# Kernel optimization log

Measured on AMD Instinct MI355X. Metric: run time of the kernel, lower is better.

Reference implementation:

```python
import jax, jax.numpy as jnp
import numpy as np

N_HEADS = 8
N_FILTERS = 512
HEAD_DIM = N_FILTERS // N_HEADS  # key_dim == value_dim == 64
BATCH = 32
SEQ = 4096


def setup_inputs() -> dict:
    key = jax.random.key(0)
    ks = jax.random.split(key, 9)
    s_in = 1.0 / np.sqrt(N_FILTERS)
    s_out = 1.0 / np.sqrt(N_HEADS * HEAD_DIM)
    return {
        "x": jax.random.normal(ks[0], (BATCH, SEQ, N_FILTERS), dtype=jnp.float32),
        # stacked per-head projection weights, stored as [H, in, out]
        "Wq": jax.random.uniform(ks[1], (N_HEADS, N_FILTERS, HEAD_DIM), jnp.float32, -s_in, s_in),
        "bq": jax.random.uniform(ks[2], (N_HEADS, HEAD_DIM), jnp.float32, -s_in, s_in),
        "Wk": jax.random.uniform(ks[3], (N_HEADS, N_FILTERS, HEAD_DIM), jnp.float32, -s_in, s_in),
        "bk": jax.random.uniform(ks[4], (N_HEADS, HEAD_DIM), jnp.float32, -s_in, s_in),
        "Wv": jax.random.uniform(ks[5], (N_HEADS, N_FILTERS, HEAD_DIM), jnp.float32, -s_in, s_in),
        "bv": jax.random.uniform(ks[6], (N_HEADS, HEAD_DIM), jnp.float32, -s_in, s_in),
        "Wo": jax.random.uniform(ks[7], (N_HEADS * HEAD_DIM, N_FILTERS), jnp.float32, -s_out, s_out),
        "bo": jax.random.uniform(ks[8], (N_FILTERS,), jnp.float32, -s_out, s_out),
    }


def reference(x, Wq, bq, Wk, bk, Wv, bv, Wo, bo):
    B, L, F = x.shape
    # Per-head projections, batched over heads: [H, B, L, D]
    Q = jnp.einsum("blf,hfd->hbld", x, Wq) + bq[:, None, None, :]
    K = jnp.einsum("blf,hfd->hbld", x, Wk) + bk[:, None, None, :]
    V = jnp.einsum("blf,hfd->hbld", x, Wv) + bv[:, None, None, :]
    # Feature-space attention: Q^T K -> [H, B, D, D], scale, softmax over dim=1 (rows)
    scores = jnp.einsum("hbld,hble->hbde", Q, K) / np.sqrt(HEAD_DIM).astype(np.float32)
    A = jax.nn.softmax(scores, axis=-2)
    # heads[i] = V @ A : [H, B, L, D]
    heads = jnp.einsum("hbld,hbde->hble", V, A)
    # Faithful to torch: heads.view(batch, l, -1) reinterprets the [H,B,L,D] buffer
    out = heads.reshape(B, L, N_HEADS * HEAD_DIM)
    return out @ Wo + bo
```

## Files before the change

kernel.cpp:

```cpp
#include <hip/hip_runtime.h>
#include <hip/hip_bf16.h>
#include <cstdint>
#include <cstddef>

#define BATCH 32
#define SEQ   4096
#define NF    512
#define NH    8
#define HD    64

typedef __bf16 bf16x8 __attribute__((ext_vector_type(8)));
typedef __bf16 bf16x4 __attribute__((ext_vector_type(4)));
typedef float  f32x4  __attribute__((ext_vector_type(4)));

__device__ __forceinline__ int lds_off(int m, int kg) {
  return (((m >> 4) * 4 + kg) * 16 + (m & 15)) * 8;
}

template<int MODE>
struct SRegs { bf16x8 h0, h1, l0, l1; };

__device__ __forceinline__ void cvt8(const float* f, bf16x8& vh, bf16x8& vl) {
#pragma unroll
  for (int j = 0; j < 8; ++j) {
    float x = f[j];
    __bf16 h = (__bf16)x;
    vh[j] = h;
    vl[j] = (__bf16)(x - (float)h);
  }
}

template<int MODE>
__device__ __forceinline__ SRegs<MODE> stage_load(
    const void* pa, const void* pb, long long zoff, int ld,
    long long row0, int k0, int tid)
{
  SRegs<MODE> R;
  if constexpr (MODE == 0 || MODE == 3) {
    const __bf16* hi = (const __bf16*)pa + zoff;
    const int r = tid >> 1, half = tid & 1;
    const size_t base = (size_t)(row0 + r) * ld + k0 + half * 16;
    R.h0 = *(const bf16x8*)(hi + base);
    R.h1 = *(const bf16x8*)(hi + base + 8);
    if constexpr (MODE == 0) {
      const __bf16* lo = (const __bf16*)pb + zoff;
      R.l0 = *(const bf16x8*)(lo + base);
      R.l1 = *(const bf16x8*)(lo + base + 8);
    }
  } else if constexpr (MODE == 1 || MODE == 4) {
    const float* A = (const float*)pa + zoff;
    const int r = tid >> 1, half = tid & 1;
    const float* src = A + (size_t)(row0 + r) * ld + k0 + half * 16;
    float f[16];
#pragma unroll
    for (int q = 0; q < 4; ++q) {
      float4 v = *(const float4*)&src[q * 4];
      f[q * 4 + 0] = v.x; f[q * 4 + 1] = v.y; f[q * 4 + 2] = v.z; f[q * 4 + 3] = v.w;
    }
    if constexpr (MODE == 1) {
      cvt8(f, R.h0, R.l0);
      cvt8(f + 8, R.h1, R.l1);
    } else {
#pragma unroll
      for (int j = 0; j < 8; ++j) {
        R.h0[j] = (__bf16)f[j];
        R.h1[j] = (__bf16)f[8 + j];
      }
    }
  } else {
    const float* A = (const float*)pa + zoff;
    const int m = tid & 127, lg = (tid >> 7) * 16;
    float f[16];
#pragma unroll
    for (int i = 0; i < 16; ++i)
      f[i] = A[(size_t)(k0 + lg + i) * ld + row0 + m];
    cvt8(f, R.h0, R.l0);
    cvt8(f + 8, R.h1, R.l1);
  }
  return R;
}

template<int MODE>
__device__ __forceinline__ void stage_store(
    const SRegs<MODE>& R, __bf16* sH, __bf16* sL, int tid)
{
  if constexpr (MODE == 2) {
    const int m = tid & 127, kq = (tid >> 7) * 2;
    *(bf16x8*)&sH[lds_off(m, kq + 0)] = R.h0;
    *(bf16x8*)&sH[lds_off(m, kq + 1)] = R.h1;
    *(bf16x8*)&sL[lds_off(m, kq + 0)] = R.l0;
    *(bf16x8*)&sL[lds_off(m, kq + 1)] = R.l1;
  } else {
    const int r = tid >> 1, kq = (tid & 1) * 2;
    *(bf16x8*)&sH[lds_off(r, kq + 0)] = R.h0;
    *(bf16x8*)&sH[lds_off(r, kq + 1)] = R.h1;
    if constexpr (MODE == 0 || MODE == 1) {
      *(bf16x8*)&sL[lds_off(r, kq + 0)] = R.l0;
      *(bf16x8*)&sL[lds_off(r, kq + 1)] = R.l1;
    }
  }
}

template<int MA, int MB, int EPI, bool SYM = false>
__global__ __launch_bounds__(256) void mfma_nt(
    const void* Aa, const void* Ab, long long sA, int lda,
    const void* Ba, const void* Bb, long long sB, int ldb,
    const float* __restrict__ bias, void* C0, void* C1, long long sC, int K)
{
  constexpr bool AL = (MA <= 2);
  constexpr bool BL = (MB <= 2);
  constexpr int NBUF = 2 + (AL ? 1 : 0) + (BL ? 1 : 0);
  __shared__ __bf16 smem[NBUF * 4096];
  __bf16* sAh = smem;
  __bf16* sBh = smem + 4096;
  __bf16* sAl = AL ? (smem + 8192) : smem;
  __bf16* sBl = BL ? (smem + (AL ? 12288 : 8192)) : smem;

  const int tid = threadIdx.x;
  const int lane = tid & 63, wave = tid >> 6;
  const int wm = wave >> 1, wn = wave & 1;

  const unsigned nx = gridDim.x, ny = gridDim.y;
  const unsigned nwg = nx * ny * gridDim.z;
  unsigned bid = blockIdx.x + nx * (blockIdx.y + ny * blockIdx.z);
  unsigned nid = (bid & 7) * (nwg >> 3) + (bid >> 3);
  const unsigned bx = nid % nx;
  unsigned t = nid / nx;
  const unsigned by = t % ny;
  const unsigned z = t / ny;

  unsigned ti = 0, tj = 0;
  long long m0;
  int n0;
  if constexpr (SYM) {
    if (bx < 4)      { ti = 0; tj = bx; }
    else if (bx < 7) { ti = 1; tj = bx - 3; }
    else if (bx < 9) { ti = 2; tj = bx - 5; }
    else             { ti = 3; tj = 3; }
    m0 = (long long)ti * 128;
    n0 = tj * 128;
  } else {
    m0 = (long long)by * 128;
    n0 = bx * 128;
  }
  const long long zA = (long long)z * sA, zB = (long long)z * sB;

  f32x4 acc[4][4];
#pragma unroll
  for (int i = 0; i < 4; ++i)
#pragma unroll
    for (int j = 0; j < 4; ++j)
#pragma unroll
      for (int c = 0; c < 4; ++c) acc[i][j][c] = 0.f;

  const int kg = lane >> 4, r = lane & 15;

  SRegs<MA> ra = stage_load<MA>(Aa, Ab, zA, lda, m0, 0, tid);
  SRegs<MB> rb = stage_load<MB>(Ba, Bb, zB, ldb, n0, 0, tid);

  for (int k0 = 0; k0 < K; k0 += 32) {
    __syncthreads();
    stage_store<MA>(ra, sAh, sAl, tid);
    stage_store<MB>(rb, sBh, sBl, tid);
    __syncthreads();
    if (k0 + 32 < K) {
      ra = stage_load<MA>(Aa, Ab, zA, lda, m0, k0 + 32, tid);
      rb = stage_load<MB>(Ba, Bb, zB, ldb, n0, k0 + 32, tid);
    }

    bf16x8 ah[4], al[4], bh[4], bl[4];
#pragma unroll
    for (int i = 0; i < 4; ++i) {
      ah[i] = *(const bf16x8*)&sAh[lds_off(wm * 64 + i * 16 + r, kg)];
      if constexpr (AL)
        al[i] = *(const bf16x8*)&sAl[lds_off(wm * 64 + i * 16 + r, kg)];
      bh[i] = *(const bf16x8*)&sBh[lds_off(wn * 64 + i * 16 + r, kg)];
      if constexpr (BL)
        bl[i] = *(const bf16x8*)&sBl[lds_off(wn * 64 + i * 16 + r, kg)];
    }
#pragma unroll
    for (int i = 0; i < 4; ++i)
#pragma unroll
      for (int j = 0; j < 4; ++j) {
        acc[i][j] = __builtin_amdgcn_mfma_f32_16x16x32_bf16(ah[i], bh[j], acc[i][j], 0, 0, 0);
        if constexpr (AL)
          acc[i][j] = __builtin_amdgcn_mfma_f32_16x16x32_bf16(al[i], bh[j], acc[i][j], 0, 0, 0);
        if constexpr (BL)
          acc[i][j] = __builtin_amdgcn_mfma_f32_16x16x32_bf16(ah[i], bl[j], acc[i][j], 0, 0, 0);
      }
  }

  const int rbase = (lane >> 4) * 4;
  const int cn = lane & 15;
#pragma unroll
  for (int i = 0; i < 4; ++i) {
    const long long gm = m0 + wm * 64 + i * 16 + rbase;
#pragma unroll
    for (int j = 0; j < 4; ++j) {
      const int gn = n0 + wn * 64 + j * 16 + cn;
      if constexpr (EPI == 0) {
        float* C = (float*)C0 + (long long)z * sC;
#pragma unroll
        for (int rr = 0; rr < 4; ++rr)
          C[(size_t)(gm + rr) * 512 + gn] = acc[i][j][rr];
      } else if constexpr (EPI == 1) {
        float* C = (float*)C0;
        const float bv = bias[gn];
#pragma unroll
        for (int rr = 0; rr < 4; ++rr)
          C[(size_t)(gm + rr) * 512 + gn] = acc[i][j][rr] + bv;
      } else if constexpr (EPI == 2) {
        __bf16* Ch = (__bf16*)C0 + (long long)z * sC;
        __bf16* Cl = (__bf16*)C1 + (long long)z * sC;
        bf16x4 th, tl;
#pragma unroll
        for (int rr = 0; rr < 4; ++rr) {
          float v = acc[i][j][rr];
          __bf16 h = (__bf16)v;
          th[rr] = h;
          tl[rr] = (__bf16)(v - (float)h);
          Ch[(size_t)(gm + rr) * 512 + gn] = h;
          Cl[(size_t)(gm + rr) * 512 + gn] = tl[rr];
        }
        if constexpr (SYM) {
          if (ti != tj) {
            *(bf16x4*)&Ch[(size_t)gn * 512 + gm] = th;
            *(bf16x4*)&Cl[(size_t)gn * 512 + gm] = tl;
          }
        }
      } else {
        const int h = gn >> 6, e = gn & 63;
        const float bv = bias[(h * 32 + (int)z) * 64 + e];
        __bf16* Ch = (__bf16*)C0;
        const size_t rowb = (size_t)(h * 32 + (int)z) * 4096 + gm;
#pragma unroll
        for (int rr = 0; rr < 4; ++rr)
          Ch[(rowb + rr) * 64 + e] = (__bf16)(acc[i][j][rr] + bv);
      }
    }
  }
}

__global__ void pack3_kernel(const float* __restrict__ Wq, const float* __restrict__ Wk,
                             const float* __restrict__ Wv, const float* __restrict__ Wo,
                             float* __restrict__ Wq_all, float* __restrict__ Wk_all,
                             float* __restrict__ Wv_all,
                             __bf16* __restrict__ Wkt_h, __bf16* __restrict__ Wkt_l,
                             __bf16* __restrict__ Wot_h) {
  int i = blockIdx.x * 256 + threadIdx.x;
  if (i >= NF * NF) return;
  int f = i >> 9, n = i & 511, h = n >> 6, d = n & 63;
  size_t src = ((size_t)h * NF + f) * HD + d;
  float wq = Wq[src], wk = Wk[src], wv = Wv[src];
  Wq_all[i] = wq;
  Wk_all[i] = wk;
  Wv_all[i] = wv;
  __bf16 kh = (__bf16)wk;
  Wkt_h[(size_t)n * 512 + f] = kh;
  Wkt_l[(size_t)n * 512 + f] = (__bf16)(wk - (float)kh);
  Wot_h[(size_t)n * 512 + f] = (__bf16)Wo[i];
}

__global__ __launch_bounds__(256) void colsum_kernel(const float* __restrict__ x,
                                                     float* __restrict__ s_part) {
  const int b = blockIdx.x, c = blockIdx.y, t = threadIdx.x;
  const float* base = x + ((size_t)b * SEQ + c * 256) * NF;
  float a0 = 0.f, a1 = 0.f;
  for (int l = 0; l < 256; ++l) {
    a0 += base[(size_t)l * NF + t];
    a1 += base[(size_t)l * NF + t + 256];
  }
  float* o = s_part + ((size_t)b * 16 + c) * NF;
  o[t] = a0;
  o[t + 256] = a1;
}

__global__ __launch_bounds__(256) void pqk_kernel(
    const float* __restrict__ s_part, const float* __restrict__ Wq_all,
    const float* __restrict__ Wk_all, float* __restrict__ pq, float* __restrict__ pk) {
  const int b = blockIdx.x, t = threadIdx.x;
  __shared__ float s[512];
  float a0 = 0.f, a1 = 0.f;
  for (int c = 0; c < 16; ++c) {
    a0 += s_part[((size_t)b * 16 + c) * NF + t];
    a1 += s_part[((size_t)b * 16 + c) * NF + t + 256];
  }
  s[t] = a0;
  s[t + 256] = a1;
  __syncthreads();
  float q0 = 0.f, q1 = 0.f, k0 = 0.f, k1 = 0.f;
  for (int f = 0; f < NF; ++f) {
    const float sv = s[f];
    q0 += sv * Wq_all[(size_t)f * NF + t];
    q1 += sv * Wq_all[(size_t)f * NF + t + 256];
    k0 += sv * Wk_all[(size_t)f * NF + t];
    k1 += sv * Wk_all[(size_t)f * NF + t + 256];
  }
  pq[(size_t)b * NF + t] = q0;
  pq[(size_t)b * NF + t + 256] = q1;
  pk[(size_t)b * NF + t] = k0;
  pk[(size_t)b * NF + t + 256] = k1;
}

__global__ __launch_bounds__(256) void score_softmax_kernel(
    const float* __restrict__ Wq_all, const float* __restrict__ U,
    const float* __restrict__ pq, const float* __restrict__ pk,
    const float* __restrict__ bq, const float* __restrict__ bk,
    const float* __restrict__ bv,
    float* __restrict__ Amat, float* __restrict__ bvA) {
  const int hb = blockIdx.x;
  const int h = hb >> 5, b = hb & 31;
  __shared__ float Qs[64][65];
  __shared__ float Us[64][65];
  __shared__ float Ss[64][65];
  __shared__ float red[4][64];
  const int tid = threadIdx.x, eg = tid & 15, dg = tid >> 4;
  const float* Ub = U + (size_t)b * NF * NF;

  float acc[4][4];
#pragma unroll
  for (int i = 0; i < 4; ++i)
#pragma unroll
    for (int j = 0; j < 4; ++j) acc[i][j] = 0.f;

  for (int f0 = 0; f0 < NF; f0 += 64) {
#pragma unroll
    for (int q = 0; q < 4; ++q) {
      const int idx = q * 256 + tid;
      const int fi = idx >> 4, dd = (idx & 15) * 4;
      *(float4*)&Qs[fi][dd] = *(const float4*)&Wq_all[(size_t)(f0 + fi) * NF + h * HD + dd];
      *(float4*)&Us[fi][dd] = *(const float4*)&Ub[(size_t)(f0 + fi) * NF + h * HD + dd];
    }
    __syncthreads();
#pragma unroll 16
    for (int fi = 0; fi < 64; ++fi) {
      float4 qa = *(float4*)&Qs[fi][dg * 4];
      float4 ub = *(float4*)&Us[fi][eg * 4];
      float qa_[4] = {qa.x, qa.y, qa.z, qa.w};
      float ub_[4] = {ub.x, ub.y, ub.z, ub.w};
#pragma unroll
      for (int i = 0; i < 4; ++i)
#pragma unroll
        for (int j = 0; j < 4; ++j) acc[i][j] = fmaf(qa_[i], ub_[j], acc[i][j]);
    }
    __syncthreads();
  }

#pragma unroll
  for (int i = 0; i < 4; ++i) {
    const int d = dg * 4 + i;
    const float bqv = bq[h * HD + d];
    const float pqv = pq[(size_t)b * NF + h * HD + d];
#pragma unroll
    for (int j = 0; j < 4; ++j) {
      const int e = eg * 4 + j;
      const float bkv = bk[h * HD + e];
      const float pkv = pk[(size_t)b * NF + h * HD + e];
      float v = acc[i][j] + bqv * pkv + bkv * pqv + 4096.f * bqv * bkv;
      Ss[d][e] = v * 0.125f;
    }
  }
  __syncthreads();

  const int e = tid & 63, q = tid >> 6;
  float pm = -INFINITY;
#pragma unroll
  for (int d = 0; d < 16; ++d) pm = fmaxf(pm, Ss[q * 16 + d][e]);
  red[q][e] = pm;
  __syncthreads();
  const float m = fmaxf(fmaxf(red[0][e], red[1][e]), fmaxf(red[2][e], red[3][e]));
  __syncthreads();
  float ps = 0.f;
#pragma unroll
  for (int d = 0; d < 16; ++d) {
    float ex = __expf(Ss[q * 16 + d][e] - m);
    Ss[q * 16 + d][e] = ex;
    ps += ex;
  }
  red[q][e] = ps;
  __syncthreads();
  const float inv = 1.f / (red[0][e] + red[1][e] + red[2][e] + red[3][e]);
  __syncthreads();
  float bacc = 0.f;
#pragma unroll
  for (int d = 0; d < 16; ++d) {
    const int dd = q * 16 + d;
    const float a = Ss[dd][e] * inv;
    Amat[(size_t)hb * 4096 + dd * 64 + e] = a;
    bacc = fmaf(bv[h * HD + dd], a, bacc);
  }
  red[q][e] = bacc;
  __syncthreads();
  if (tid < 64)
    bvA[(size_t)hb * HD + tid] = red[0][tid] + red[1][tid] + red[2][tid] + red[3][tid];
}

__global__ __launch_bounds__(256) void wva_kernel(
    const float* __restrict__ Wv_all, const float* __restrict__ Amat,
    __bf16* __restrict__ WvAt_h) {
  const int hb = blockIdx.y, h = hb >> 5, b = hb & 31;
  const int f0 = blockIdx.x * 128;
  __shared__ float Ws[128][65];
  __shared__ float As[64][65];
  const int tid = threadIdx.x;

#pragma unroll
  for (int q = 0; q < 4; ++q) {
    const int idx = q * 256 + tid;
    const int d = idx >> 4, ee = (idx & 15) * 4;
    *(float4*)&As[d][ee] = *(const float4*)&Amat[(size_t)hb * 4096 + d * 64 + ee];
  }
#pragma unroll
  for (int q = 0; q < 8; ++q) {
    const int idx = q * 256 + tid;
    const int fi = idx >> 4, dd = (idx & 15) * 4;
    *(float4*)&Ws[fi][dd] = *(const float4*)&Wv_all[(size_t)(f0 + fi) * NF + h * HD + dd];
  }
  __syncthreads();

  const int fg = tid >> 4, eg = tid & 15;
  float acc[8][4];
#pragma unroll
  for (int i = 0; i < 8; ++i)
#pragma unroll
    for (int j = 0; j < 4; ++j) acc[i][j] = 0.f;
#pragma unroll 8
  for (int d = 0; d < 64; ++d) {
    float4 av = *(float4*)&As[d][eg * 4];
    float a_[4] = {av.x, av.y, av.z, av.w};
#pragma unroll
    for (int i = 0; i < 8; ++i) {
      const float w = Ws[fg * 8 + i][d];
#pragma unroll
      for (int j = 0; j < 4; ++j) acc[i][j] = fmaf(w, a_[j], acc[i][j]);
    }
  }

  __syncthreads();
  float* Ts = &Ws[0][0];
#pragma unroll
  for (int i = 0; i < 8; ++i)
#pragma unroll
    for (int j = 0; j < 4; ++j)
      Ts[(eg * 4 + j) * 130 + fg * 8 + i] = acc[i][j];
  __syncthreads();

  const int e = tid >> 2, fs = (tid & 3) * 32;
  size_t orow = ((size_t)b * 512 + h * 64 + e) * 512 + f0 + fs;
#pragma unroll
  for (int c = 0; c < 4; ++c) {
    bf16x8 vh;
#pragma unroll
    for (int j = 0; j < 8; ++j)
      vh[j] = (__bf16)Ts[e * 130 + fs + c * 8 + j];
    *(bf16x8*)&WvAt_h[orow + c * 8] = vh;
  }
}

extern "C" void kernel_launch(void* const* d_in, const int* in_sizes, int n_in,
                              void* d_out, int out_size, void* d_ws, size_t ws_size,
                              hipStream_t stream) {
  const float* x  = (const float*)d_in[0];
  const float* Wq = (const float*)d_in[1];
  const float* bq = (const float*)d_in[2];
  const float* Wk = (const float*)d_in[3];
  const float* bk = (const float*)d_in[4];
  const float* Wv = (const float*)d_in[5];
  const float* bv = (const float*)d_in[6];
  const float* Wo = (const float*)d_in[7];
  const float* bo = (const float*)d_in[8];
  float* out = (float*)d_out;
  (void)in_sizes; (void)n_in; (void)out_size; (void)ws_size;

  float* w = (float*)d_ws;
  size_t off = 0;
  float* Wq_all = w + off; off += 262144;
  float* Wk_all = w + off; off += 262144;
  float* Wv_all = w + off; off += 262144;
  float* s_part = w + off; off += 262144;
  float* pq     = w + off; off += 16384;
  float* pk     = w + off; off += 16384;
  float* U      = w + off; off += (size_t)32 * 262144;
  float* Amat   = w + off; off += 1048576;
  float* bvA    = w + off; off += 16384;
  __bf16* Wkt_h = (__bf16*)(w + off); off += 131072;
  __bf16* Wkt_l = (__bf16*)(w + off); off += 131072;
  __bf16* Wot_h = (__bf16*)(w + off); off += 131072;
  __bf16* Gh    = (__bf16*)(w + off); off += (size_t)32 * 131072;
  __bf16* Gl    = (__bf16*)(w + off); off += (size_t)32 * 131072;
  __bf16* WvAt_h= (__bf16*)(w + off); off += (size_t)32 * 131072;
  __bf16* Hh    = (__bf16*)(w + off); off += (size_t)131072 * 256;

  pack3_kernel<<<1024, 256, 0, stream>>>(Wq, Wk, Wv, Wo, Wq_all, Wk_all, Wv_all,
                                         Wkt_h, Wkt_l, Wot_h);
  colsum_kernel<<<dim3(BATCH, 16), 256, 0, stream>>>(x, s_part);
  pqk_kernel<<<BATCH, 256, 0, stream>>>(s_part, Wq_all, Wk_all, pq, pk);
  mfma_nt<2, 2, 2, true><<<dim3(10, 1, BATCH), 256, 0, stream>>>(
      x, nullptr, (long long)SEQ * NF, NF,
      x, nullptr, (long long)SEQ * NF, NF,
      nullptr, Gh, Gl, 262144, SEQ);
  mfma_nt<0, 0, 0><<<dim3(4, 4, BATCH), 256, 0, stream>>>(
      Gh, Gl, 262144, NF,
      Wkt_h, Wkt_l, 0, NF,
      nullptr, U, nullptr, 262144, NF);
  score_softmax_kernel<<<256, 256, 0, stream>>>(Wq_all, U, pq, pk, bq, bk, bv,
                                                Amat, bvA);
  wva_kernel<<<dim3(4, 256), 256, 0, stream>>>(Wv_all, Amat, WvAt_h);
  mfma_nt<4, 3, 3><<<dim3(4, 32, BATCH), 256, 0, stream>>>(
      x, nullptr, (long long)SEQ * NF, NF,
      WvAt_h, nullptr, 262144, NF,
      bvA, Hh, nullptr, 0, NF);
  mfma_nt<3, 3, 1><<<dim3(4, 1024, 1), 256, 0, stream>>>(
      Hh, nullptr, 0, NF,
      Wot_h, nullptr, 0, NF,
      bo, out, nullptr, 0, NF);
}
```

Baseline: 1.085 ms.

## Split-K the Gram matrix GEMM over sequence and add reduction kernel

The symmetric x^T x Gram GEMM previously ran only 10x32 workgroups, each looping over the full 4096-long sequence. It now splits K four ways (gridDim.y=4) and writes fp32 partial tiles to a workspace. A new greduce kernel sums the partials, splits them into bf16 hi/lo, and writes the mirrored transpose tiles. The column-sum kernel also gets more parallelism: 64 chunks instead of 16. Both changes trade extra workspace traffic and an extra launch for better GPU occupancy.

```diff
diff --git a/kernel.cpp b/kernel.cpp
--- a/kernel.cpp
+++ b/kernel.cpp
@@ -132,6 +132,7 @@
   unsigned ti = 0, tj = 0;
   long long m0;
   int n0;
+  int kbase = 0;
   if constexpr (SYM) {
     if (bx < 4)      { ti = 0; tj = bx; }
     else if (bx < 7) { ti = 1; tj = bx - 3; }
@@ -139,6 +140,7 @@
     else             { ti = 3; tj = 3; }
     m0 = (long long)ti * 128;
     n0 = tj * 128;
+    kbase = (int)by * K;
   } else {
     m0 = (long long)by * 128;
     n0 = bx * 128;
@@ -155,15 +157,16 @@
 
   const int kg = lane >> 4, r = lane & 15;
 
-  SRegs<MA> ra = stage_load<MA>(Aa, Ab, zA, lda, m0, 0, tid);
-  SRegs<MB> rb = stage_load<MB>(Ba, Bb, zB, ldb, n0, 0, tid);
-
-  for (int k0 = 0; k0 < K; k0 += 32) {
+  SRegs<MA> ra = stage_load<MA>(Aa, Ab, zA, lda, m0, kbase, tid);
+  SRegs<MB> rb = stage_load<MB>(Ba, Bb, zB, ldb, n0, kbase, tid);
+
+  const int kend = kbase + K;
+  for (int k0 = kbase; k0 < kend; k0 += 32) {
     __syncthreads();
     stage_store<MA>(ra, sAh, sAl, tid);
     stage_store<MB>(rb, sBh, sBl, tid);
     __syncthreads();
-    if (k0 + 32 < K) {
+    if (k0 + 32 < kend) {
       ra = stage_load<MA>(Aa, Ab, zA, lda, m0, k0 + 32, tid);
       rb = stage_load<MB>(Ba, Bb, zB, ldb, n0, k0 + 32, tid);
     }
@@ -195,9 +198,11 @@
 #pragma unroll
   for (int i = 0; i < 4; ++i) {
     const long long gm = m0 + wm * 64 + i * 16 + rbase;
+    const int lm = wm * 64 + i * 16 + rbase;
 #pragma unroll
     for (int j = 0; j < 4; ++j) {
       const int gn = n0 + wn * 64 + j * 16 + cn;
+      const int ln = wn * 64 + j * 16 + cn;
       if constexpr (EPI == 0) {
         float* C = (float*)C0 + (long long)z * sC;
 #pragma unroll
@@ -209,26 +214,7 @@
 #pragma unroll
         for (int rr = 0; rr < 4; ++rr)
           C[(size_t)(gm + rr) * 512 + gn] = acc[i][j][rr] + bv;
-      } else if constexpr (EPI == 2) {
-        __bf16* Ch = (__bf16*)C0 + (long long)z * sC;
-        __bf16* Cl = (__bf16*)C1 + (long long)z * sC;
-        bf16x4 th, tl;
-#pragma unroll
-        for (int rr = 0; rr < 4; ++rr) {
-          float v = acc[i][j][rr];
-          __bf16 h = (__bf16)v;
-          th[rr] = h;
-          tl[rr] = (__bf16)(v - (float)h);
-          Ch[(size_t)(gm + rr) * 512 + gn] = h;
-          Cl[(size_t)(gm + rr) * 512 + gn] = tl[rr];
-        }
-        if constexpr (SYM) {
-          if (ti != tj) {
-            *(bf16x4*)&Ch[(size_t)gn * 512 + gm] = th;
-            *(bf16x4*)&Cl[(size_t)gn * 512 + gm] = tl;
-          }
-        }
-      } else {
+      } else if constexpr (EPI == 3) {
         const int h = gn >> 6, e = gn & 63;
         const float bv = bias[(h * 32 + (int)z) * 64 + e];
         __bf16* Ch = (__bf16*)C0;
@@ -236,7 +222,57 @@
 #pragma unroll
         for (int rr = 0; rr < 4; ++rr)
           Ch[(rowb + rr) * 64 + e] = (__bf16)(acc[i][j][rr] + bv);
+      } else {
+        float* C = (float*)C0 + ((((long long)by * 32 + z) * 10 + bx) * 16384);
+#pragma unroll
+        for (int rr = 0; rr < 4; ++rr)
+          C[(size_t)(lm + rr) * 128 + ln] = acc[i][j][rr];
       }
+    }
+  }
+}
+
+__global__ __launch_bounds__(256) void greduce_kernel(
+    const float* __restrict__ Gp, __bf16* __restrict__ Gh,
+    __bf16* __restrict__ Gl) {
+  const int t = blockIdx.x, z = blockIdx.y;
+  const int tid = threadIdx.x;
+  __shared__ float T[128][129];
+  int ti, tj;
+  if (t < 4)      { ti = 0; tj = t; }
+  else if (t < 7) { ti = 1; tj = t - 3; }
+  else if (t < 9) { ti = 2; tj = t - 5; }
+  else            { ti = 3; tj = 3; }
+  const size_t base = ((size_t)z * 10 + t) * 16384;
+  const size_t cstep = (size_t)32 * 10 * 16384;
+#pragma unroll 4
+  for (int i = 0; i < 64; ++i) {
+    const int idx = i * 256 + tid;
+    float v = Gp[base + idx] + Gp[base + cstep + idx]
+            + Gp[base + 2 * cstep + idx] + Gp[base + 3 * cstep + idx];
+    T[idx >> 7][idx & 127] = v;
+  }
+  __syncthreads();
+  __bf16* GhZ = Gh + (size_t)z * 262144;
+  __bf16* GlZ = Gl + (size_t)z * 262144;
+#pragma unroll 4
+  for (int i = 0; i < 64; ++i) {
+    const int idx = i * 256 + tid;
+    const int lm = idx >> 7, ln = idx & 127;
+    const float v = T[lm][ln];
+    const __bf16 h = (__bf16)v;
+    GhZ[(size_t)(ti * 128 + lm) * 512 + tj * 128 + ln] = h;
+    GlZ[(size_t)(ti * 128 + lm) * 512 + tj * 128 + ln] = (__bf16)(v - (float)h);
+  }
+  if (ti != tj) {
+#pragma unroll 4
+    for (int i = 0; i < 64; ++i) {
+      const int idx = i * 256 + tid;
+      const int q = idx >> 7, p = idx & 127;
+      const float v = T[p][q];
+      const __bf16 h = (__bf16)v;
+      GhZ[(size_t)(tj * 128 + q) * 512 + ti * 128 + p] = h;
+      GlZ[(size_t)(tj * 128 + q) * 512 + ti * 128 + p] = (__bf16)(v - (float)h);
     }
   }
 }
@@ -264,13 +300,13 @@
 __global__ __launch_bounds__(256) void colsum_kernel(const float* __restrict__ x,
                                                      float* __restrict__ s_part) {
   const int b = blockIdx.x, c = blockIdx.y, t = threadIdx.x;
-  const float* base = x + ((size_t)b * SEQ + c * 256) * NF;
+  const float* base = x + ((size_t)b * SEQ + c * 64) * NF;
   float a0 = 0.f, a1 = 0.f;
-  for (int l = 0; l < 256; ++l) {
+  for (int l = 0; l < 64; ++l) {
     a0 += base[(size_t)l * NF + t];
     a1 += base[(size_t)l * NF + t + 256];
   }
-  float* o = s_part + ((size_t)b * 16 + c) * NF;
+  float* o = s_part + ((size_t)b * 64 + c) * NF;
   o[t] = a0;
   o[t + 256] = a1;
 }
@@ -281,9 +317,9 @@
   const int b = blockIdx.x, t = threadIdx.x;
   __shared__ float s[512];
   float a0 = 0.f, a1 = 0.f;
-  for (int c = 0; c < 16; ++c) {
-    a0 += s_part[((size_t)b * 16 + c) * NF + t];
-    a1 += s_part[((size_t)b * 16 + c) * NF + t + 256];
+  for (int c = 0; c < 64; ++c) {
+    a0 += s_part[((size_t)b * 64 + c) * NF + t];
+    a1 += s_part[((size_t)b * 64 + c) * NF + t + 256];
   }
   s[t] = a0;
   s[t + 256] = a1;
@@ -477,12 +513,13 @@
   float* Wq_all = w + off; off += 262144;
   float* Wk_all = w + off; off += 262144;
   float* Wv_all = w + off; off += 262144;
-  float* s_part = w + off; off += 262144;
+  float* s_part = w + off; off += (size_t)32 * 64 * 512;
   float* pq     = w + off; off += 16384;
   float* pk     = w + off; off += 16384;
   float* U      = w + off; off += (size_t)32 * 262144;
   float* Amat   = w + off; off += 1048576;
   float* bvA    = w + off; off += 16384;
+  float* Gp     = w + off; off += (size_t)4 * 32 * 10 * 16384;
   __bf16* Wkt_h = (__bf16*)(w + off); off += 131072;
   __bf16* Wkt_l = (__bf16*)(w + off); off += 131072;
   __bf16* Wot_h = (__bf16*)(w + off); off += 131072;
@@ -493,12 +530,13 @@
 
   pack3_kernel<<<1024, 256, 0, stream>>>(Wq, Wk, Wv, Wo, Wq_all, Wk_all, Wv_all,
                                          Wkt_h, Wkt_l, Wot_h);
-  colsum_kernel<<<dim3(BATCH, 16), 256, 0, stream>>>(x, s_part);
+  colsum_kernel<<<dim3(BATCH, 64), 256, 0, stream>>>(x, s_part);
   pqk_kernel<<<BATCH, 256, 0, stream>>>(s_part, Wq_all, Wk_all, pq, pk);
-  mfma_nt<2, 2, 2, true><<<dim3(10, 1, BATCH), 256, 0, stream>>>(
+  mfma_nt<2, 2, 4, true><<<dim3(10, 4, BATCH), 256, 0, stream>>>(
       x, nullptr, (long long)SEQ * NF, NF,
       x, nullptr, (long long)SEQ * NF, NF,
-      nullptr, Gh, Gl, 262144, SEQ);
+      nullptr, Gp, nullptr, 0, 1024);
+  greduce_kernel<<<dim3(10, BATCH), 256, 0, stream>>>(Gp, Gh, Gl);
   mfma_nt<0, 0, 0><<<dim3(4, 4, BATCH), 256, 0, stream>>>(
       Gh, Gl, 262144, NF,
       Wkt_h, Wkt_l, 0, NF,
```

New measurement: 1.047 ms. 1.04x faster.
